# Kernel optimization log

Hardware: AMD Instinct MI355X
Metric: run time of the kernel (lower is better)

Reference implementation:

```python
import jax, jax.numpy as jnp
import numpy as np

VAR_WEIGHT = 1.0
DIST_WEIGHT = 1.0
MARGIN_VAR = 0.5
MARGIN_DIST = 3.0
IGNORE_LABEL = 255
MAX_INST = 12  # static C: max instance id present in gt (labels 1..12, 0=background)


def setup_inputs() -> dict:
    key = jax.random.key(0)
    k1, k2 = jax.random.split(key)
    featmap = jax.random.normal(k1, (8, 16, 368, 640), dtype=jnp.float32)
    gt = jax.random.randint(k2, (8, 1, 368, 640), 0, 13, dtype=jnp.int64)
    return {"featmap": featmap, "gt": gt}


def _push_pull_loss(featmap, gt):
    B, N, H, W = featmap.shape
    P = H * W
    feat = featmap.reshape(B, N, P)                      # [B,N,P]
    labels = gt.reshape(B, P)                            # [B,P] int
    ids = jnp.arange(1, MAX_INST + 1)                    # instance ids 1..C
    # one-hot instance masks  [B,C,P]
    mask = (labels[:, None, :] == ids[None, :, None]).astype(feat.dtype)
    counts = mask.sum(axis=-1)                           # [B,C]
    present = counts > 0                                 # [B,C]
    safe_counts = jnp.maximum(counts, 1.0)
    # per-instance centers (segment mean)  [B,C,N]
    centers = jnp.einsum('bnp,bcp->bcn', feat, mask) / safe_counts[:, :, None]

    # --- pull: per-pixel distance to own-instance center ---
    feat_sq = jnp.sum(feat * feat, axis=1)               # [B,P]
    cen_sq = jnp.sum(centers * centers, axis=-1)         # [B,C]
    cross = jnp.einsum('bcn,bnp->bcp', centers, feat)    # [B,C,P]
    sq = feat_sq[:, None, :] + cen_sq[:, :, None] - 2.0 * cross
    sq = jnp.maximum(sq, 0.0)
    d = jnp.where(sq > 0, jnp.sqrt(jnp.where(sq > 0, sq, 1.0)), 0.0)  # [B,C,P]
    hinge = jnp.maximum(d - MARGIN_VAR, 0.0)
    # per-instance mean over its own pixels
    inst_pull = jnp.sum(hinge * mask, axis=-1) / safe_counts          # [B,C]
    n_inst = jnp.sum(present.astype(feat.dtype))
    pull_loss = jnp.where(
        n_inst > 0,
        jnp.sum(jnp.where(present, inst_pull, 0.0)) / jnp.maximum(n_inst, 1.0),
        0.0 * feat.mean(),
    ) * VAR_WEIGHT

    # --- push: pairwise center distances within each batch sample ---
    diff = centers[:, :, None, :] - centers[:, None, :, :]            # [B,C,C,N]
    psq = jnp.sum(diff * diff, axis=-1)                               # [B,C,C]
    pd = jnp.where(psq > 0, jnp.sqrt(jnp.where(psq > 0, psq, 1.0)), 0.0)
    pair_valid = (present[:, :, None] & present[:, None, :] &
                  (~jnp.eye(MAX_INST, dtype=bool))[None]).astype(feat.dtype)
    push_vals = jnp.maximum(2.0 * MARGIN_DIST - pd, 0.0)
    n_pairs = jnp.sum(pair_valid)
    push_loss = jnp.where(
        n_pairs > 0,
        jnp.sum(push_vals * pair_valid) / jnp.maximum(n_pairs, 1.0),
        0.0 * feat.mean(),
    ) * DIST_WEIGHT

    return push_loss + pull_loss


def reference(featmap, gt):
    return _push_pull_loss(featmap, gt)
```

## Files before the change

kernel.cpp:

```cpp
#include <hip/hip_runtime.h>
#include <hip/hip_bf16.h>

constexpr int B_ = 8;
constexpr int N_ = 16;
constexpr int H_ = 368;
constexpr int W_ = 640;
constexpr int P_ = H_ * W_;
constexpr int C_ = 12;
constexpr float MARGIN_VAR_ = 0.5f;
constexpr float MARGIN_DIST_ = 3.0f;

constexpr int OFF_SUMS = 0;
constexpr int OFF_CNT  = OFF_SUMS + B_*C_*N_;
constexpr int WS_FLOATS = OFF_CNT + B_*C_;

constexpr int TPB = 256;

constexpr int ACH   = 1024;
constexpr int APAIR = 2 * ACH;
constexpr int ABPI  = P_ / APAIR;
constexpr int PCHUNK = 1024;
constexpr int PBPI   = P_ / PCHUNK;
constexpr int NBLK   = B_ * PBPI;

constexpr int RS = 1048;

typedef short bf16x8 __attribute__((ext_vector_type(8)));
typedef float f32x4  __attribute__((ext_vector_type(4)));

union FragU { int4 i; bf16x8 v; };

__device__ __forceinline__ short f2bf(float f) {
    __hip_bfloat16 h = __float2bfloat16(f);
    return __builtin_bit_cast(short, h);
}

__device__ __forceinline__ int pack_bf2(float x, float y) {
    const unsigned lo = (unsigned short)f2bf(x);
    const unsigned hi = (unsigned short)f2bf(y);
    return (int)(lo | (hi << 16));
}

__global__ __launch_bounds__(TPB) void k_accum(const float* __restrict__ feat,
                                               const int* __restrict__ gt,
                                               float* __restrict__ ws,
                                               float* __restrict__ out) {
    __shared__ int   s_lab[2][ACH];
    __shared__ short s_feat[N_ * RS];
    __shared__ float s_red[4][C_];

    const int tid  = threadIdx.x;
    const int lane = tid & 63, wid = tid >> 6;
    const int b    = blockIdx.x / ABPI;
    const int pair = blockIdx.x % ABPI;
    const int base = pair * APAIR;

    if (blockIdx.x == 0 && tid == 0) out[0] = 0.f;

    const int*   __restrict__ gb = gt   + (size_t)b * P_ + base;
    const float* __restrict__ fb = feat + (size_t)b * N_ * P_ + base;

    const int4 lab0 = ((const int4*)gb)[tid];
    const int4 lab1 = ((const int4*)gb)[256 + tid];
    float4 tr[16];
    #pragma unroll
    for (int j = 0; j < 16; ++j)
        tr[j] = *(const float4*)(fb + (size_t)j * P_ + tid * 4);

    ((int4*)&s_lab[0][0])[tid] = lab0;
    ((int4*)&s_lab[1][0])[tid] = lab1;

    float cnt[C_];
    #pragma unroll
    for (int c = 0; c < C_; ++c) {
        cnt[c] = ((lab0.x == c+1) ? 1.f : 0.f) + ((lab0.y == c+1) ? 1.f : 0.f)
               + ((lab0.z == c+1) ? 1.f : 0.f) + ((lab0.w == c+1) ? 1.f : 0.f)
               + ((lab1.x == c+1) ? 1.f : 0.f) + ((lab1.y == c+1) ? 1.f : 0.f)
               + ((lab1.z == c+1) ? 1.f : 0.f) + ((lab1.w == c+1) ? 1.f : 0.f);
    }
    #pragma unroll
    for (int off = 32; off > 0; off >>= 1) {
        #pragma unroll
        for (int c = 0; c < C_; ++c) cnt[c] += __shfl_xor(cnt[c], off, 64);
    }
    if (lane == 0) {
        #pragma unroll
        for (int c = 0; c < C_; ++c) s_red[wid][c] = cnt[c];
    }

    #pragma unroll
    for (int j = 0; j < 16; ++j) {
        const float4 v = tr[j];
        tr[j] = *(const float4*)(fb + (size_t)j * P_ + ACH + tid * 4);
        int2 w; w.x = pack_bf2(v.x, v.y); w.y = pack_bf2(v.z, v.w);
        *(int2*)(s_feat + j * RS + tid * 4) = w;
    }
    __syncthreads();

    if (tid < C_) {
        const float t = s_red[0][tid] + s_red[1][tid] + s_red[2][tid] + s_red[3][tid];
        atomicAdd(&ws[OFF_CNT + b * C_ + tid], t);
    }

    const int n   = lane & 15;
    const int cls = n + 1;
    const int ko  = (lane >> 4) * 8;

    f32x4 acc = {0.f, 0.f, 0.f, 0.f};

    #pragma unroll
    for (int k = 0; k < 8; ++k) {
        const int t = wid * 8 + k;
        const int* lp = &s_lab[0][0] + t * 32 + ko;
        const int4 L0 = *(const int4*)(lp);
        const int4 L1 = *(const int4*)(lp + 4);
        FragU au, bu;
        au.i.x = ((L0.x == cls) ? 0x3F80 : 0) | ((L0.y == cls) ? 0x3F800000 : 0);
        au.i.y = ((L0.z == cls) ? 0x3F80 : 0) | ((L0.w == cls) ? 0x3F800000 : 0);
        au.i.z = ((L1.x == cls) ? 0x3F80 : 0) | ((L1.y == cls) ? 0x3F800000 : 0);
        au.i.w = ((L1.z == cls) ? 0x3F80 : 0) | ((L1.w == cls) ? 0x3F800000 : 0);
        bu.v = *(const bf16x8*)(s_feat + n * RS + t * 32 + ko);
        acc = __builtin_amdgcn_mfma_f32_16x16x32_bf16(au.v, bu.v, acc, 0, 0, 0);
    }
    __syncthreads();

    #pragma unroll
    for (int j = 0; j < 16; ++j) {
        int2 w; w.x = pack_bf2(tr[j].x, tr[j].y); w.y = pack_bf2(tr[j].z, tr[j].w);
        *(int2*)(s_feat + j * RS + tid * 4) = w;
    }
    __syncthreads();

    #pragma unroll
    for (int k = 0; k < 8; ++k) {
        const int t = wid * 8 + k;
        const int* lp = &s_lab[1][0] + t * 32 + ko;
        const int4 L0 = *(const int4*)(lp);
        const int4 L1 = *(const int4*)(lp + 4);
        FragU au, bu;
        au.i.x = ((L0.x == cls) ? 0x3F80 : 0) | ((L0.y == cls) ? 0x3F800000 : 0);
        au.i.y = ((L0.z == cls) ? 0x3F80 : 0) | ((L0.w == cls) ? 0x3F800000 : 0);
        au.i.z = ((L1.x == cls) ? 0x3F80 : 0) | ((L1.y == cls) ? 0x3F800000 : 0);
        au.i.w = ((L1.z == cls) ? 0x3F80 : 0) | ((L1.w == cls) ? 0x3F800000 : 0);
        bu.v = *(const bf16x8*)(s_feat + n * RS + t * 32 + ko);
        acc = __builtin_amdgcn_mfma_f32_16x16x32_bf16(au.v, bu.v, acc, 0, 0, 0);
    }

    float* s_fin = (float*)&s_lab[0][0];
    #pragma unroll
    for (int r = 0; r < 4; ++r) s_fin[wid * 256 + lane * 4 + r] = acc[r];
    __syncthreads();
    {
        const float sv = s_fin[0 * 256 + tid] + s_fin[1 * 256 + tid]
                       + s_fin[2 * 256 + tid] + s_fin[3 * 256 + tid];
        const int elane = tid >> 2, r = tid & 3;
        const int row = (elane >> 4) * 4 + r;
        const int col = elane & 15;
        if (row < C_)
            atomicAdd(&ws[OFF_SUMS + ((size_t)b * C_ + row) * N_ + col], sv);
    }
}

__global__ __launch_bounds__(TPB) void k_pull(const float* __restrict__ feat,
                                              const int* __restrict__ gt,
                                              const float* __restrict__ ws,
                                              float* __restrict__ out) {
    __shared__ float s_cen[C_][N_ + 1];
    __shared__ float s_w[C_];
    __shared__ float s_cntv[B_ * C_];
    __shared__ float red[TPB];
    __shared__ float wsum[TPB / 64];

    const int tid = threadIdx.x;
    const int g2    = (NBLK / 8 - 1 - (int)(blockIdx.x >> 3)) * 8 + (blockIdx.x & 7);
    const int b     = g2 / PBPI;
    const int chunk = g2 % PBPI;
    const int base  = chunk * PCHUNK;

    const float* __restrict__ fbase = feat + (size_t)b * N_ * P_ + base + tid * 4;

    const int4 lb = *(const int4*)(gt + (size_t)b * P_ + base + tid * 4);
    float4 va[4], vb[4];
    #pragma unroll
    for (int j = 0; j < 4; ++j) va[j] = *(const float4*)(fbase + (size_t)(j) * P_);
    #pragma unroll
    for (int j = 0; j < 4; ++j) vb[j] = *(const float4*)(fbase + (size_t)(4 + j) * P_);

    if (tid < B_ * C_) s_cntv[tid] = ws[OFF_CNT + tid];
    __syncthreads();

    float n_inst = 0.f;
    #pragma unroll 8
    for (int i = 0; i < B_ * C_; ++i) n_inst += (s_cntv[i] > 0.f) ? 1.f : 0.f;

    if (tid < C_ * N_) {
        const int c = tid >> 4, n = tid & 15;
        const float ct = s_cntv[b * C_ + c];
        s_cen[c][n] = ws[OFF_SUMS + ((size_t)b * C_ + c) * N_ + n] / fmaxf(ct, 1.f);
    }
    if (tid < C_) {
        const float ct = s_cntv[b * C_ + tid];
        s_w[tid] = (ct > 0.f && n_inst > 0.f) ? 1.0f / (ct * n_inst) : 0.f;
    }
    __syncthreads();

    if (chunk == 0) {
        float ps = 0.f;
        if (tid < C_ * C_) {
            const int i = tid / C_, j = tid % C_;
            if (i != j && s_cntv[b * C_ + i] > 0.f && s_cntv[b * C_ + j] > 0.f) {
                float sq = 0.f;
                #pragma unroll
                for (int n = 0; n < N_; ++n) {
                    const float d = s_cen[i][n] - s_cen[j][n];
                    sq += d * d;
                }
                ps = fmaxf(2.f * MARGIN_DIST_ - sqrtf(sq), 0.f);
            }
        }
        red[tid] = ps;
        __syncthreads();
        for (int s = TPB / 2; s > 0; s >>= 1) {
            if (tid < s) red[tid] += red[tid + s];
            __syncthreads();
        }
        if (tid == 0) {
            float np = 0.f;
            for (int bb_ = 0; bb_ < B_; ++bb_) {
                int k = 0;
                for (int c = 0; c < C_; ++c) k += (s_cntv[bb_ * C_ + c] > 0.f) ? 1 : 0;
                np += (float)(k * (k - 1));
            }
            if (np > 0.f) atomicAdd(out, red[0] / np);
        }
    }

    const bool vx = (lb.x >= 1 && lb.x <= C_);
    const bool vy = (lb.y >= 1 && lb.y <= C_);
    const bool vz = (lb.z >= 1 && lb.z <= C_);
    const bool vw = (lb.w >= 1 && lb.w <= C_);
    const int cx = vx ? lb.x - 1 : 0;
    const int cy = vy ? lb.y - 1 : 0;
    const int cz = vz ? lb.z - 1 : 0;
    const int cw = vw ? lb.w - 1 : 0;

    float sq0 = 0.f, sq1 = 0.f, sq2 = 0.f, sq3 = 0.f;

    auto consume4 = [&](const float4* r, int cb) {
        #pragma unroll
        for (int j = 0; j < 4; ++j) {
            const int nn = cb + j;
            const float d0 = r[j].x - s_cen[cx][nn];
            const float d1 = r[j].y - s_cen[cy][nn];
            const float d2 = r[j].z - s_cen[cz][nn];
            const float d3 = r[j].w - s_cen[cw][nn];
            sq0 += d0 * d0; sq1 += d1 * d1; sq2 += d2 * d2; sq3 += d3 * d3;
        }
    };

    consume4(va, 0);
    #pragma unroll
    for (int j = 0; j < 4; ++j) va[j] = *(const float4*)(fbase + (size_t)(8 + j) * P_);
    consume4(vb, 4);
    #pragma unroll
    for (int j = 0; j < 4; ++j) vb[j] = *(const float4*)(fbase + (size_t)(12 + j) * P_);
    consume4(va, 8);
    consume4(vb, 12);

    float acc = 0.f;
    acc += fmaxf(sqrtf(sq0) - MARGIN_VAR_, 0.f) * (vx ? s_w[cx] : 0.f);
    acc += fmaxf(sqrtf(sq1) - MARGIN_VAR_, 0.f) * (vy ? s_w[cy] : 0.f);
    acc += fmaxf(sqrtf(sq2) - MARGIN_VAR_, 0.f) * (vz ? s_w[cz] : 0.f);
    acc += fmaxf(sqrtf(sq3) - MARGIN_VAR_, 0.f) * (vw ? s_w[cw] : 0.f);

    #pragma unroll
    for (int off = 32; off > 0; off >>= 1) acc += __shfl_down(acc, off, 64);
    const int lane = tid & 63, wid = tid >> 6;
    if (lane == 0) wsum[wid] = acc;
    __syncthreads();
    if (tid == 0) {
        float t = 0.f;
        #pragma unroll
        for (int w = 0; w < TPB / 64; ++w) t += wsum[w];
        atomicAdd(out, t);
    }
}

extern "C" void kernel_launch(void* const* d_in, const int* in_sizes, int n_in,
                              void* d_out, int out_size, void* d_ws, size_t ws_size,
                              hipStream_t stream) {
    const float* feat = (const float*)d_in[0];
    const int*   gt   = (const int*)d_in[1];
    float* out = (float*)d_out;
    float* ws  = (float*)d_ws;

    (void)hipMemsetAsync(d_ws, 0, WS_FLOATS * sizeof(float), stream);

    k_accum<<<dim3(B_ * ABPI), dim3(TPB), 0, stream>>>(feat, gt, ws, out);
    k_pull <<<dim3(NBLK), dim3(TPB), 0, stream>>>(feat, gt, ws, out);
}
```

Measured before the change: 64.97 us.

## Process two pixel chunks per pull block and pack labels to bytes in shared memory

The pull kernel now handles two 1024-pixel chunks per block, halving the grid. It keeps a rolling prefetch of feature rows across both chunks, which amortises the per-block setup (loading counts, centers and weights) and keeps more loads in flight. The accumulate kernel packs labels into bytes in shared memory, which cuts LDS traffic for building the one-hot MFMA operands, and gives the final reduction its own shared buffer. The risks are fewer blocks to fill the GPU and higher register pressure from the longer unrolled code.

```diff
diff --git a/kernel.cpp b/kernel.cpp
--- a/kernel.cpp
+++ b/kernel.cpp
@@ -19,9 +19,10 @@
 constexpr int ACH   = 1024;
 constexpr int APAIR = 2 * ACH;
 constexpr int ABPI  = P_ / APAIR;
-constexpr int PCHUNK = 1024;
-constexpr int PBPI   = P_ / PCHUNK;
-constexpr int NBLK   = B_ * PBPI;
+constexpr int PCH   = 1024;
+constexpr int PPAIR = 2 * PCH;
+constexpr int PBPI  = P_ / PPAIR;
+constexpr int PNB   = B_ * PBPI;
 
 constexpr int RS = 1048;
 
@@ -45,9 +46,10 @@
                                                const int* __restrict__ gt,
                                                float* __restrict__ ws,
                                                float* __restrict__ out) {
-    __shared__ int   s_lab[2][ACH];
+    __shared__ int   s_lab8[APAIR / 4];
     __shared__ short s_feat[N_ * RS];
     __shared__ float s_red[4][C_];
+    __shared__ float s_fin[1024];
 
     const int tid  = threadIdx.x;
     const int lane = tid & 63, wid = tid >> 6;
@@ -67,8 +69,8 @@
     for (int j = 0; j < 16; ++j)
         tr[j] = *(const float4*)(fb + (size_t)j * P_ + tid * 4);
 
-    ((int4*)&s_lab[0][0])[tid] = lab0;
-    ((int4*)&s_lab[1][0])[tid] = lab1;
+    s_lab8[tid]       = lab0.x | (lab0.y << 8) | (lab0.z << 16) | (lab0.w << 24);
+    s_lab8[256 + tid] = lab1.x | (lab1.y << 8) | (lab1.z << 16) | (lab1.w << 24);
 
     float cnt[C_];
     #pragma unroll
@@ -103,7 +105,7 @@
     }
 
     const int n   = lane & 15;
-    const int cls = n + 1;
+    const unsigned cls = (unsigned)(n + 1);
     const int ko  = (lane >> 4) * 8;
 
     f32x4 acc = {0.f, 0.f, 0.f, 0.f};
@@ -111,14 +113,13 @@
     #pragma unroll
     for (int k = 0; k < 8; ++k) {
         const int t = wid * 8 + k;
-        const int* lp = &s_lab[0][0] + t * 32 + ko;
-        const int4 L0 = *(const int4*)(lp);
-        const int4 L1 = *(const int4*)(lp + 4);
+        const int2 L = *(const int2*)(s_lab8 + t * 8 + (ko >> 2));
+        const unsigned u0 = (unsigned)L.x, u1 = (unsigned)L.y;
         FragU au, bu;
-        au.i.x = ((L0.x == cls) ? 0x3F80 : 0) | ((L0.y == cls) ? 0x3F800000 : 0);
-        au.i.y = ((L0.z == cls) ? 0x3F80 : 0) | ((L0.w == cls) ? 0x3F800000 : 0);
-        au.i.z = ((L1.x == cls) ? 0x3F80 : 0) | ((L1.y == cls) ? 0x3F800000 : 0);
-        au.i.w = ((L1.z == cls) ? 0x3F80 : 0) | ((L1.w == cls) ? 0x3F800000 : 0);
+        au.i.x = (((u0      ) & 0xFF) == cls ? 0x3F80 : 0) | (((u0 >>  8) & 0xFF) == cls ? 0x3F800000 : 0);
+        au.i.y = (((u0 >> 16) & 0xFF) == cls ? 0x3F80 : 0) | (((u0 >> 24)       ) == cls ? 0x3F800000 : 0);
+        au.i.z = (((u1      ) & 0xFF) == cls ? 0x3F80 : 0) | (((u1 >>  8) & 0xFF) == cls ? 0x3F800000 : 0);
+        au.i.w = (((u1 >> 16) & 0xFF) == cls ? 0x3F80 : 0) | (((u1 >> 24)       ) == cls ? 0x3F800000 : 0);
         bu.v = *(const bf16x8*)(s_feat + n * RS + t * 32 + ko);
         acc = __builtin_amdgcn_mfma_f32_16x16x32_bf16(au.v, bu.v, acc, 0, 0, 0);
     }
@@ -134,19 +135,17 @@
     #pragma unroll
     for (int k = 0; k < 8; ++k) {
         const int t = wid * 8 + k;
-        const int* lp = &s_lab[1][0] + t * 32 + ko;
-        const int4 L0 = *(const int4*)(lp);
-        const int4 L1 = *(const int4*)(lp + 4);
+        const int2 L = *(const int2*)(s_lab8 + 256 + t * 8 + (ko >> 2));
+        const unsigned u0 = (unsigned)L.x, u1 = (unsigned)L.y;
         FragU au, bu;
-        au.i.x = ((L0.x == cls) ? 0x3F80 : 0) | ((L0.y == cls) ? 0x3F800000 : 0);
-        au.i.y = ((L0.z == cls) ? 0x3F80 : 0) | ((L0.w == cls) ? 0x3F800000 : 0);
-        au.i.z = ((L1.x == cls) ? 0x3F80 : 0) | ((L1.y == cls) ? 0x3F800000 : 0);
-        au.i.w = ((L1.z == cls) ? 0x3F80 : 0) | ((L1.w == cls) ? 0x3F800000 : 0);
+        au.i.x = (((u0      ) & 0xFF) == cls ? 0x3F80 : 0) | (((u0 >>  8) & 0xFF) == cls ? 0x3F800000 : 0);
+        au.i.y = (((u0 >> 16) & 0xFF) == cls ? 0x3F80 : 0) | (((u0 >> 24)       ) == cls ? 0x3F800000 : 0);
+        au.i.z = (((u1      ) & 0xFF) == cls ? 0x3F80 : 0) | (((u1 >>  8) & 0xFF) == cls ? 0x3F800000 : 0);
+        au.i.w = (((u1 >> 16) & 0xFF) == cls ? 0x3F80 : 0) | (((u1 >> 24)       ) == cls ? 0x3F800000 : 0);
         bu.v = *(const bf16x8*)(s_feat + n * RS + t * 32 + ko);
         acc = __builtin_amdgcn_mfma_f32_16x16x32_bf16(au.v, bu.v, acc, 0, 0, 0);
     }
 
-    float* s_fin = (float*)&s_lab[0][0];
     #pragma unroll
     for (int r = 0; r < 4; ++r) s_fin[wid * 256 + lane * 4 + r] = acc[r];
     __syncthreads();
@@ -172,19 +171,22 @@
     __shared__ float wsum[TPB / 64];
 
     const int tid = threadIdx.x;
-    const int g2    = (NBLK / 8 - 1 - (int)(blockIdx.x >> 3)) * 8 + (blockIdx.x & 7);
-    const int b     = g2 / PBPI;
-    const int chunk = g2 % PBPI;
-    const int base  = chunk * PCHUNK;
-
-    const float* __restrict__ fbase = feat + (size_t)b * N_ * P_ + base + tid * 4;
-
-    const int4 lb = *(const int4*)(gt + (size_t)b * P_ + base + tid * 4);
+    const int g2   = (PNB / 8 - 1 - (int)(blockIdx.x >> 3)) * 8 + (blockIdx.x & 7);
+    const int b    = g2 / PBPI;
+    const int pair = g2 % PBPI;
+    const int base = pair * PPAIR;
+
+    const int*   __restrict__ gb = gt + (size_t)b * P_ + base;
+    const float* __restrict__ f0 = feat + (size_t)b * N_ * P_ + base + tid * 4;
+    const float* __restrict__ f1 = f0 + PCH;
+
+    const int4 lb0 = ((const int4*)gb)[tid];
+    const int4 lb1 = ((const int4*)gb)[256 + tid];
     float4 va[4], vb[4];
     #pragma unroll
-    for (int j = 0; j < 4; ++j) va[j] = *(const float4*)(fbase + (size_t)(j) * P_);
-    #pragma unroll
-    for (int j = 0; j < 4; ++j) vb[j] = *(const float4*)(fbase + (size_t)(4 + j) * P_);
+    for (int j = 0; j < 4; ++j) va[j] = *(const float4*)(f0 + (size_t)j * P_);
+    #pragma unroll
+    for (int j = 0; j < 4; ++j) vb[j] = *(const float4*)(f0 + (size_t)(4 + j) * P_);
 
     if (tid < B_ * C_) s_cntv[tid] = ws[OFF_CNT + tid];
     __syncthreads();
@@ -204,7 +206,7 @@
     }
     __syncthreads();
 
-    if (chunk == 0) {
+    if (pair == 0) {
         float ps = 0.f;
         if (tid < C_ * C_) {
             const int i = tid / C_, j = tid % C_;
@@ -235,48 +237,116 @@
         }
     }
 
-    const bool vx = (lb.x >= 1 && lb.x <= C_);
-    const bool vy = (lb.y >= 1 && lb.y <= C_);
-    const bool vz = (lb.z >= 1 && lb.z <= C_);
-    const bool vw = (lb.w >= 1 && lb.w <= C_);
-    const int cx = vx ? lb.x - 1 : 0;
-    const int cy = vy ? lb.y - 1 : 0;
-    const int cz = vz ? lb.z - 1 : 0;
-    const int cw = vw ? lb.w - 1 : 0;
-
-    float sq0 = 0.f, sq1 = 0.f, sq2 = 0.f, sq3 = 0.f;
-
-    auto consume4 = [&](const float4* r, int cb) {
-        #pragma unroll
-        for (int j = 0; j < 4; ++j) {
-            const int nn = cb + j;
-            const float d0 = r[j].x - s_cen[cx][nn];
-            const float d1 = r[j].y - s_cen[cy][nn];
-            const float d2 = r[j].z - s_cen[cz][nn];
-            const float d3 = r[j].w - s_cen[cw][nn];
-            sq0 += d0 * d0; sq1 += d1 * d1; sq2 += d2 * d2; sq3 += d3 * d3;
-        }
-    };
-
-    consume4(va, 0);
-    #pragma unroll
-    for (int j = 0; j < 4; ++j) va[j] = *(const float4*)(fbase + (size_t)(8 + j) * P_);
-    consume4(vb, 4);
-    #pragma unroll
-    for (int j = 0; j < 4; ++j) vb[j] = *(const float4*)(fbase + (size_t)(12 + j) * P_);
-    consume4(va, 8);
-    consume4(vb, 12);
-
-    float acc = 0.f;
-    acc += fmaxf(sqrtf(sq0) - MARGIN_VAR_, 0.f) * (vx ? s_w[cx] : 0.f);
-    acc += fmaxf(sqrtf(sq1) - MARGIN_VAR_, 0.f) * (vy ? s_w[cy] : 0.f);
-    acc += fmaxf(sqrtf(sq2) - MARGIN_VAR_, 0.f) * (vz ? s_w[cz] : 0.f);
-    acc += fmaxf(sqrtf(sq3) - MARGIN_VAR_, 0.f) * (vw ? s_w[cw] : 0.f);
-
-    #pragma unroll
-    for (int off = 32; off > 0; off >>= 1) acc += __shfl_down(acc, off, 64);
+    float accv = 0.f;
+
+    {
+        const bool vx = (lb0.x >= 1 && lb0.x <= C_);
+        const bool vy = (lb0.y >= 1 && lb0.y <= C_);
+        const bool vz = (lb0.z >= 1 && lb0.z <= C_);
+        const bool vw = (lb0.w >= 1 && lb0.w <= C_);
+        const int cx = vx ? lb0.x - 1 : 0;
+        const int cy = vy ? lb0.y - 1 : 0;
+        const int cz = vz ? lb0.z - 1 : 0;
+        const int cw = vw ? lb0.w - 1 : 0;
+
+        float sq0 = 0.f, sq1 = 0.f, sq2 = 0.f, sq3 = 0.f;
+
+        #pragma unroll
+        for (int j = 0; j < 4; ++j) {
+            const float4 r = va[j];
+            va[j] = *(const float4*)(f0 + (size_t)(8 + j) * P_);
+            const float d0 = r.x - s_cen[cx][j],     d1 = r.y - s_cen[cy][j];
+            const float d2 = r.z - s_cen[cz][j],     d3 = r.w - s_cen[cw][j];
+            sq0 += d0*d0; sq1 += d1*d1; sq2 += d2*d2; sq3 += d3*d3;
+        }
+        #pragma unroll
+        for (int j = 0; j < 4; ++j) {
+            const float4 r = vb[j];
+            vb[j] = *(const float4*)(f0 + (size_t)(12 + j) * P_);
+            const int nn = 4 + j;
+            const float d0 = r.x - s_cen[cx][nn],    d1 = r.y - s_cen[cy][nn];
+            const float d2 = r.z - s_cen[cz][nn],    d3 = r.w - s_cen[cw][nn];
+            sq0 += d0*d0; sq1 += d1*d1; sq2 += d2*d2; sq3 += d3*d3;
+        }
+        #pragma unroll
+        for (int j = 0; j < 4; ++j) {
+            const float4 r = va[j];
+            va[j] = *(const float4*)(f1 + (size_t)j * P_);
+            const int nn = 8 + j;
+            const float d0 = r.x - s_cen[cx][nn],    d1 = r.y - s_cen[cy][nn];
+            const float d2 = r.z - s_cen[cz][nn],    d3 = r.w - s_cen[cw][nn];
+            sq0 += d0*d0; sq1 += d1*d1; sq2 += d2*d2; sq3 += d3*d3;
+        }
+        #pragma unroll
+        for (int j = 0; j < 4; ++j) {
+            const float4 r = vb[j];
+            vb[j] = *(const float4*)(f1 + (size_t)(4 + j) * P_);
+            const int nn = 12 + j;
+            const float d0 = r.x - s_cen[cx][nn],    d1 = r.y - s_cen[cy][nn];
+            const float d2 = r.z - s_cen[cz][nn],    d3 = r.w - s_cen[cw][nn];
+            sq0 += d0*d0; sq1 += d1*d1; sq2 += d2*d2; sq3 += d3*d3;
+        }
+        accv += fmaxf(sqrtf(sq0) - MARGIN_VAR_, 0.f) * (vx ? s_w[cx] : 0.f);
+        accv += fmaxf(sqrtf(sq1) - MARGIN_VAR_, 0.f) * (vy ? s_w[cy] : 0.f);
+        accv += fmaxf(sqrtf(sq2) - MARGIN_VAR_, 0.f) * (vz ? s_w[cz] : 0.f);
+        accv += fmaxf(sqrtf(sq3) - MARGIN_VAR_, 0.f) * (vw ? s_w[cw] : 0.f);
+    }
+
+    {
+        const bool vx = (lb1.x >= 1 && lb1.x <= C_);
+        const bool vy = (lb1.y >= 1 && lb1.y <= C_);
+        const bool vz = (lb1.z >= 1 && lb1.z <= C_);
+        const bool vw = (lb1.w >= 1 && lb1.w <= C_);
+        const int cx = vx ? lb1.x - 1 : 0;
+        const int cy = vy ? lb1.y - 1 : 0;
+        const int cz = vz ? lb1.z - 1 : 0;
+        const int cw = vw ? lb1.w - 1 : 0;
+
+        float sq0 = 0.f, sq1 = 0.f, sq2 = 0.f, sq3 = 0.f;
+
+        #pragma unroll
+        for (int j = 0; j < 4; ++j) {
+            const float4 r = va[j];
+            va[j] = *(const float4*)(f1 + (size_t)(8 + j) * P_);
+            const float d0 = r.x - s_cen[cx][j],     d1 = r.y - s_cen[cy][j];
+            const float d2 = r.z - s_cen[cz][j],     d3 = r.w - s_cen[cw][j];
+            sq0 += d0*d0; sq1 += d1*d1; sq2 += d2*d2; sq3 += d3*d3;
+        }
+        #pragma unroll
+        for (int j = 0; j < 4; ++j) {
+            const float4 r = vb[j];
+            vb[j] = *(const float4*)(f1 + (size_t)(12 + j) * P_);
+            const int nn = 4 + j;
+            const float d0 = r.x - s_cen[cx][nn],    d1 = r.y - s_cen[cy][nn];
+            const float d2 = r.z - s_cen[cz][nn],    d3 = r.w - s_cen[cw][nn];
+            sq0 += d0*d0; sq1 += d1*d1; sq2 += d2*d2; sq3 += d3*d3;
+        }
+        #pragma unroll
+        for (int j = 0; j < 4; ++j) {
+            const float4 r = va[j];
+            const int nn = 8 + j;
+            const float d0 = r.x - s_cen[cx][nn],    d1 = r.y - s_cen[cy][nn];
+            const float d2 = r.z - s_cen[cz][nn],    d3 = r.w - s_cen[cw][nn];
+            sq0 += d0*d0; sq1 += d1*d1; sq2 += d2*d2; sq3 += d3*d3;
+        }
+        #pragma unroll
+        for (int j = 0; j < 4; ++j) {
+            const float4 r = vb[j];
+            const int nn = 12 + j;
+            const float d0 = r.x - s_cen[cx][nn],    d1 = r.y - s_cen[cy][nn];
+            const float d2 = r.z - s_cen[cz][nn],    d3 = r.w - s_cen[cw][nn];
+            sq0 += d0*d0; sq1 += d1*d1; sq2 += d2*d2; sq3 += d3*d3;
+        }
+        accv += fmaxf(sqrtf(sq0) - MARGIN_VAR_, 0.f) * (vx ? s_w[cx] : 0.f);
+        accv += fmaxf(sqrtf(sq1) - MARGIN_VAR_, 0.f) * (vy ? s_w[cy] : 0.f);
+        accv += fmaxf(sqrtf(sq2) - MARGIN_VAR_, 0.f) * (vz ? s_w[cz] : 0.f);
+        accv += fmaxf(sqrtf(sq3) - MARGIN_VAR_, 0.f) * (vw ? s_w[cw] : 0.f);
+    }
+
+    #pragma unroll
+    for (int off = 32; off > 0; off >>= 1) accv += __shfl_down(accv, off, 64);
     const int lane = tid & 63, wid = tid >> 6;
-    if (lane == 0) wsum[wid] = acc;
+    if (lane == 0) wsum[wid] = accv;
     __syncthreads();
     if (tid == 0) {
         float t = 0.f;
@@ -297,5 +367,5 @@
     (void)hipMemsetAsync(d_ws, 0, WS_FLOATS * sizeof(float), stream);
 
     k_accum<<<dim3(B_ * ABPI), dim3(TPB), 0, stream>>>(feat, gt, ws, out);
-    k_pull <<<dim3(NBLK), dim3(TPB), 0, stream>>>(feat, gt, ws, out);
-}
+    k_pull <<<dim3(PNB), dim3(TPB), 0, stream>>>(feat, gt, ws, out);
+}
```

After: 59.44 us. 8.5% less time.
